# Kernel tuning notes

Hardware: AMD Instinct MI355X
Metric: run time of the kernel (lower is better)

Reference implementation:

```python
import jax, jax.numpy as jnp
import numpy as np

B, E, H, V, D2, T = 128, 512, 512, 32000, 1024, 17

def setup_inputs() -> dict:
    key = jax.random.key(0)
    ks = jax.random.split(key, 13)
    s = 0.02
    return {
        "features": jax.random.normal(ks[0], (B, 512), dtype=jnp.float32),
        "captions": jax.random.randint(ks[1], (B, T), 0, V, dtype=jnp.int32),
        "W_enc": jax.random.normal(ks[2], (512, E), dtype=jnp.float32) * s,
        "b_enc": jnp.zeros((E,), dtype=jnp.float32),
        "emb": jax.random.normal(ks[3], (V, E), dtype=jnp.float32) * s,
        "W_ih": jax.random.normal(ks[4], (4 * H, E), dtype=jnp.float32) * s,
        "b_ih": jnp.zeros((4 * H,), dtype=jnp.float32),
        "W_hh": jax.random.normal(ks[5], (4 * H, H), dtype=jnp.float32) * s,
        "b_hh": jnp.zeros((4 * H,), dtype=jnp.float32),
        "W_d2": jax.random.normal(ks[6], (H, D2), dtype=jnp.float32) * s,
        "b_d2": jnp.zeros((D2,), dtype=jnp.float32),
        "W_last": jax.random.normal(ks[7], (D2, V), dtype=jnp.float32) * s,
        "b_last": jnp.zeros((V,), dtype=jnp.float32),
    }


def reference(features, captions, W_enc, b_enc, emb, W_ih, b_ih, W_hh, b_hh, W_d2, b_d2, W_last, b_last):
    # encoder_last: project frozen-resnet features [B,512] -> [B,E]
    feat = features @ W_enc + b_enc
    # embed captions[:, :-1] -> [B,16,E], prepend image feature -> [B,17,E]
    e = emb[captions[:, :-1]]
    x = jnp.concatenate([feat[:, None, :], e], axis=1)  # [B,T,E]

    def step(carry, xt):
        h, c = carry
        gates = xt @ W_ih.T + b_ih + h @ W_hh.T + b_hh  # [B,4H]
        i, f, g, o = jnp.split(gates, 4, axis=-1)  # PyTorch LSTMCell gate order
        i, f, o = jax.nn.sigmoid(i), jax.nn.sigmoid(f), jax.nn.sigmoid(o)
        g = jnp.tanh(g)
        c = f * c + i * g
        h = o * jnp.tanh(c)
        return (h, c), h

    h0 = jnp.zeros((x.shape[0], H), dtype=x.dtype)
    c0 = jnp.zeros((x.shape[0], H), dtype=x.dtype)
    _, hs = jax.lax.scan(step, (h0, c0), jnp.swapaxes(x, 0, 1))  # [T,B,H]
    hs = jnp.swapaxes(hs, 0, 1)  # [B,T,H]

    out = jax.nn.relu(hs @ W_d2 + b_d2)       # [B,T,D2]
    logits = out @ W_last + b_last            # [B,T,V]
    return jax.nn.softmax(logits, axis=2)
```

## Files before the change

### kernel.cpp

```cpp
#include <hip/hip_runtime.h>
#include <hip/hip_bf16.h>

#define B_   128
#define T_   17
#define E_   512
#define H_   512
#define V_   32000
#define D2_  1024
#define MR_  (B_*T_)

typedef __attribute__((ext_vector_type(8))) short short8;
typedef __attribute__((ext_vector_type(4))) float f32x4;

__device__ __forceinline__ unsigned short f2b(float f) {
  unsigned u = __float_as_uint(f);
  u += 0x7FFFu + ((u >> 16) & 1u);
  return (unsigned short)(u >> 16);
}
__device__ __forceinline__ float sigf(float x) { return 1.f / (1.f + __expf(-x)); }
__device__ __forceinline__ float tanhfast(float x) {
  x = fminf(fmaxf(x, -15.f), 15.f);
  float e = __expf(2.f * x);
  return (e - 1.f) / (e + 1.f);
}

__device__ __forceinline__ void async16(const void* g, void* l) {
  __builtin_amdgcn_global_load_lds((const __attribute__((address_space(1))) unsigned int*)g,
                                   (__attribute__((address_space(3))) unsigned int*)l,
                                   16, 0, 0);
}

template<int EPI>
__global__ __launch_bounds__(256, 2)
void gemm_bt(const unsigned short* __restrict__ A,
             const unsigned short* __restrict__ Bt,
             void* __restrict__ C,
             const float* __restrict__ bias0,
             const float* __restrict__ bias1,
             int N, int K)
{
  __shared__ unsigned short sA[128 * 32];
  __shared__ unsigned short sB[128 * 32];

  const int tid  = threadIdx.x;
  const int lane = tid & 63;
  const int wave = tid >> 6;
  const int wm   = wave & 1;
  const int wn   = wave >> 1;
  const size_t bm = (size_t)blockIdx.x * 128;
  const size_t bn = (size_t)blockIdx.y * 128;

  const int sRow   = wave * 32 + (lane >> 2);
  const int gchunk = (lane & 3) ^ ((sRow >> 2) & 3);

  const unsigned short* gA  = A  + (bm + sRow)      * (size_t)K + gchunk * 8;
  const unsigned short* gA2 = A  + (bm + sRow + 16) * (size_t)K + gchunk * 8;
  const unsigned short* gB  = Bt + (bn + sRow)      * (size_t)K + gchunk * 8;
  const unsigned short* gB2 = Bt + (bn + sRow + 16) * (size_t)K + gchunk * 8;

  unsigned short* lA  = &sA[wave * 1024];
  unsigned short* lA2 = &sA[wave * 1024 + 512];
  unsigned short* lB  = &sB[wave * 1024];
  unsigned short* lB2 = &sB[wave * 1024 + 512];

  f32x4 acc[4][4] = {};
  const int fm = lane & 15;
  const int q  = lane >> 4;

  for (int kt = 0; kt < K; kt += 32) {
    async16(gA  + kt, lA);
    async16(gA2 + kt, lA2);
    async16(gB  + kt, lB);
    async16(gB2 + kt, lB2);
    __syncthreads();

    short8 af[4], bfv[4];
#pragma unroll
    for (int i = 0; i < 4; i++) {
      int ra = wm * 64 + i * 16 + fm;
      af[i]  = *(const short8*)&sA[ra * 32 + ((q ^ ((ra >> 2) & 3)) * 8)];
      int rb = wn * 64 + i * 16 + fm;
      bfv[i] = *(const short8*)&sB[rb * 32 + ((q ^ ((rb >> 2) & 3)) * 8)];
    }
#pragma unroll
    for (int i = 0; i < 4; i++)
#pragma unroll
      for (int j = 0; j < 4; j++)
        acc[i][j] = __builtin_amdgcn_mfma_f32_16x16x32_bf16(af[i], bfv[j], acc[i][j], 0, 0, 0);
    __syncthreads();
  }

#pragma unroll
  for (int i = 0; i < 4; i++) {
#pragma unroll
    for (int j = 0; j < 4; j++) {
      size_t col = bn + wn * 64 + j * 16 + fm;
      float bv = 0.f;
      if constexpr (EPI == 0) {
        size_t oc = ((col & 3) << 9) + (col >> 2);
        bv = bias0[oc] + bias1[oc];
      }
      if constexpr (EPI == 2 || EPI == 3 || EPI == 4) bv = bias0[col];
#pragma unroll
      for (int r = 0; r < 4; r++) {
        size_t row = bm + wm * 64 + i * 16 + q * 4 + r;
        float v = acc[i][j][r] + bv;
        if constexpr (EPI == 2) {
          v = v > 0.f ? v : 0.f;
          ((unsigned short*)C)[row * N + col] = f2b(v);
        } else if constexpr (EPI == 3) {
          ((unsigned short*)C)[row * N + col] = f2b(v);
        } else {
          ((float*)C)[row * N + col] = v;
        }
      }
    }
  }
}

__global__ __launch_bounds__(256)
void lstm_step(const unsigned short* __restrict__ hprev,
               const unsigned short* __restrict__ Whh,
               const float* __restrict__ Gt,
               float* __restrict__ c,
               unsigned short* __restrict__ hout,
               unsigned short* __restrict__ hsb,
               int t)
{
  __shared__ float gl[128 * 132];
  unsigned short* sA = (unsigned short*)gl;
  unsigned short* sB = (unsigned short*)(gl + 4096);

  const int tid  = threadIdx.x;
  const int lane = tid & 63;
  const int wave = tid >> 6;
  const int wm   = wave & 1;
  const int wn   = wave >> 1;
  const int n0   = blockIdx.x * 128;

  const int sR  = lane >> 3;
  const int gch = (lane & 7) ^ sR;
  const size_t aoff = (size_t)(wave * 32 + sR) * 512 + gch * 8;
  const size_t boff = (size_t)(n0 + wave * 32 + sR) * 512 + gch * 8;

  f32x4 acc[4][4] = {};
  const int fm = lane & 15;
  const int q  = lane >> 4;

  for (int kt = 0; kt < 512; kt += 64) {
#pragma unroll
    for (int s = 0; s < 4; s++) {
      async16(hprev + aoff + s * 4096 + kt, sA + wave * 2048 + s * 512);
      async16(Whh   + boff + s * 4096 + kt, sB + wave * 2048 + s * 512);
    }
    __syncthreads();

    short8 af[2][4], bfv[2][4];
#pragma unroll
    for (int kk = 0; kk < 2; kk++) {
      int cch = kk * 4 + q;
#pragma unroll
      for (int i = 0; i < 4; i++) {
        int ra = wm * 64 + i * 16 + fm;
        af[kk][i]  = *(const short8*)&sA[ra * 64 + ((cch ^ (ra & 7)) * 8)];
        int rb = wn * 64 + i * 16 + fm;
        bfv[kk][i] = *(const short8*)&sB[rb * 64 + ((cch ^ (rb & 7)) * 8)];
      }
    }
#pragma unroll
    for (int kk = 0; kk < 2; kk++)
#pragma unroll
      for (int i = 0; i < 4; i++)
#pragma unroll
        for (int j = 0; j < 4; j++)
          acc[i][j] = __builtin_amdgcn_mfma_f32_16x16x32_bf16(af[kk][i], bfv[kk][j], acc[i][j], 0, 0, 0);
    __syncthreads();
  }

#pragma unroll
  for (int i = 0; i < 4; i++)
#pragma unroll
    for (int j = 0; j < 4; j++)
#pragma unroll
      for (int r = 0; r < 4; r++)
        gl[(wm * 64 + i * 16 + q * 4 + r) * 132 + wn * 64 + j * 16 + fm] = acc[i][j][r];
  __syncthreads();

#pragma unroll
  for (int it = 0; it < 16; it++) {
    int p   = it * 256 + tid;
    int row = p >> 5;
    int ul  = p & 31;
    float4 a4 = *(float4*)&gl[row * 132 + ul * 4];
    float4 G4 = *(const float4*)&Gt[row * 2048 + n0 + ul * 4];
    float gi = a4.x + G4.x, gf = a4.y + G4.y, gg = a4.z + G4.z, go = a4.w + G4.w;
    int gu  = (n0 >> 2) + ul;
    int idx = row * 512 + gu;
    float cn = sigf(gf) * c[idx] + sigf(gi) * tanhfast(gg);
    c[idx] = cn;
    float hn = sigf(go) * tanhfast(cn);
    unsigned short h16 = f2b(hn);
    hout[idx] = h16;
    hsb[((size_t)row * T_ + t) * 512 + gu] = h16;
  }
}

__global__ void lstm_point0(const float* __restrict__ G0, float* __restrict__ c,
                            unsigned short* __restrict__ hb, unsigned short* __restrict__ hsb) {
  int idx = blockIdx.x * 256 + threadIdx.x;
  int b = idx >> 9, u = idx & 511;
  float4 g4 = ((const float4*)(G0 + (size_t)b * 2048))[u];
  float cn = sigf(g4.x) * tanhfast(g4.z);
  c[idx] = cn;
  float hn = sigf(g4.w) * tanhfast(cn);
  unsigned short h16 = f2b(hn);
  hb[idx] = h16;
  hsb[((size_t)b * T_ + 0) * 512 + u] = h16;
}

__global__ void permute_cvt(const float* __restrict__ src, unsigned short* __restrict__ dst) {
  int p  = blockIdx.x;
  int ir = ((p & 3) << 9) + (p >> 2);
  float4 v = ((const float4*)(src + (size_t)ir * 512))[threadIdx.x];
  ushort4 o;
  o.x = f2b(v.x); o.y = f2b(v.y); o.z = f2b(v.z); o.w = f2b(v.w);
  ((ushort4*)(dst + (size_t)p * 512))[threadIdx.x] = o;
}

__global__ void transpose_cvt(const float* __restrict__ src, unsigned short* __restrict__ dst,
                              int K, int N) {
  __shared__ float tile[32][33];
  int n0 = blockIdx.x * 32, k0 = blockIdx.y * 32;
  int tcol = threadIdx.x & 31, trow = threadIdx.x >> 5;
  for (int r = trow; r < 32; r += 8)
    tile[r][tcol] = src[(size_t)(k0 + r) * N + n0 + tcol];
  __syncthreads();
  for (int r = trow; r < 32; r += 8)
    dst[(size_t)(n0 + r) * K + k0 + tcol] = f2b(tile[tcol][r]);
}

__global__ __launch_bounds__(256) void encode(const float* __restrict__ features,
                                              const float* __restrict__ W_enc,
                                              const float* __restrict__ b_enc,
                                              unsigned short* __restrict__ xb) {
  __shared__ float fs[512];
  int b = blockIdx.y, e = blockIdx.x * 256 + threadIdx.x;
  fs[threadIdx.x]       = features[b * 512 + threadIdx.x];
  fs[threadIdx.x + 256] = features[b * 512 + threadIdx.x + 256];
  __syncthreads();
  float acc = 0.f;
#pragma unroll 8
  for (int k = 0; k < 512; k++) acc += fs[k] * W_enc[(size_t)k * 512 + e];
  xb[(size_t)b * 512 + e] = f2b(acc + b_enc[e]);
}

__global__ void embed_k(const int* __restrict__ captions, const float* __restrict__ emb,
                        unsigned short* __restrict__ xb) {
  int t = blockIdx.x + 1, b = blockIdx.y;
  int tok = captions[b * T_ + (t - 1)];
  float4 v = ((const float4*)(emb + (size_t)tok * 512))[threadIdx.x];
  ushort4 o;
  o.x = f2b(v.x); o.y = f2b(v.y); o.z = f2b(v.z); o.w = f2b(v.w);
  ((ushort4*)(xb + (size_t)(t * B_ + b) * 512))[threadIdx.x] = o;
}

__global__ __launch_bounds__(1024) void softmax_b(const unsigned short* __restrict__ lg,
                                                  float* __restrict__ out) {
  __shared__ float ps[1024];
  const uint4* r4 = (const uint4*)(lg + (size_t)blockIdx.x * V_);
  float* orow = out + (size_t)blockIdx.x * V_;
  int tid = threadIdx.x;
  float v[4][8];
  float s = 0.f;
#pragma unroll
  for (int u = 0; u < 4; u++) {
    int i = u * 1024 + tid;
    if (i < 4000) {
      uint4 w = r4[i];
      unsigned a[4] = {w.x, w.y, w.z, w.w};
#pragma unroll
      for (int k = 0; k < 4; k++) {
        float lo = __uint_as_float(a[k] << 16);
        float hi = __uint_as_float(a[k] & 0xffff0000u);
        float e0 = __expf(lo), e1 = __expf(hi);
        v[u][2 * k] = e0; v[u][2 * k + 1] = e1;
        s += e0 + e1;
      }
    }
  }
  ps[tid] = s;
  __syncthreads();
  for (int o = 512; o > 0; o >>= 1) {
    if (tid < o) ps[tid] += ps[tid + o];
    __syncthreads();
  }
  float inv = 1.f / ps[0];
#pragma unroll
  for (int u = 0; u < 4; u++) {
    int i = u * 1024 + tid;
    if (i < 4000) {
      float4 o1 = {v[u][0] * inv, v[u][1] * inv, v[u][2] * inv, v[u][3] * inv};
      float4 o2 = {v[u][4] * inv, v[u][5] * inv, v[u][6] * inv, v[u][7] * inv};
      ((float4*)(orow + (size_t)i * 8))[0] = o1;
      ((float4*)(orow + (size_t)i * 8))[1] = o2;
    }
  }
}

__global__ __launch_bounds__(1024) void softmax_f(float* __restrict__ out) {
  __shared__ float ps[1024];
  float* r = out + (size_t)blockIdx.x * V_;
  int tid = threadIdx.x;
  float v[32];
  float s = 0.f;
#pragma unroll
  for (int u = 0; u < 32; u++) {
    int i = u * 1024 + tid;
    if (i < V_) { float e = __expf(r[i]); v[u] = e; s += e; }
  }
  ps[tid] = s;
  __syncthreads();
  for (int o = 512; o > 0; o >>= 1) {
    if (tid < o) ps[tid] += ps[tid + o];
    __syncthreads();
  }
  float inv = 1.f / ps[0];
#pragma unroll
  for (int u = 0; u < 32; u++) {
    int i = u * 1024 + tid;
    if (i < V_) r[i] = v[u] * inv;
  }
}

extern "C" void kernel_launch(void* const* d_in, const int* in_sizes, int n_in,
                              void* d_out, int out_size, void* d_ws, size_t ws_size,
                              hipStream_t stream) {
  const float* features = (const float*)d_in[0];
  const int*   captions = (const int*)d_in[1];
  const float* W_enc  = (const float*)d_in[2];
  const float* b_enc  = (const float*)d_in[3];
  const float* emb    = (const float*)d_in[4];
  const float* W_ih   = (const float*)d_in[5];
  const float* b_ih   = (const float*)d_in[6];
  const float* W_hh   = (const float*)d_in[7];
  const float* b_hh   = (const float*)d_in[8];
  const float* W_d2   = (const float*)d_in[9];
  const float* b_d2   = (const float*)d_in[10];
  const float* W_last = (const float*)d_in[11];
  const float* b_last = (const float*)d_in[12];
  float* out = (float*)d_out;

  char* ws = (char*)d_ws;
  size_t off = 0;
  auto alloc = [&](size_t bytes) -> void* {
    void* p = ws + off;
    off += (bytes + 255) & ~(size_t)255;
    return p;
  };
  unsigned short* xb     = (unsigned short*)alloc((size_t)MR_ * E_ * 2);
  unsigned short* Wb_ih  = (unsigned short*)alloc((size_t)4 * H_ * E_ * 2);
  unsigned short* Wb_hh  = (unsigned short*)alloc((size_t)4 * H_ * H_ * 2);
  unsigned short* Wb_d2t = (unsigned short*)alloc((size_t)D2_ * H_ * 2);
  unsigned short* Wb_lt  = (unsigned short*)alloc((size_t)V_ * D2_ * 2);
  float*          G      = (float*)alloc((size_t)MR_ * 4 * H_ * 4);
  float*          cst    = (float*)alloc((size_t)B_ * H_ * 4);
  unsigned short* hb0    = (unsigned short*)alloc((size_t)B_ * H_ * 2);
  unsigned short* hb1    = (unsigned short*)alloc((size_t)B_ * H_ * 2);
  unsigned short* hsb    = (unsigned short*)alloc((size_t)MR_ * H_ * 2);
  unsigned short* outb   = (unsigned short*)alloc((size_t)MR_ * D2_ * 2);
  size_t off_base = off;
  unsigned short* lgb    = (unsigned short*)alloc((size_t)MR_ * V_ * 2);
  const bool bf16_logits = (off <= ws_size);
  (void)in_sizes; (void)n_in; (void)out_size; (void)off_base;

  permute_cvt<<<2048, 128, 0, stream>>>(W_ih, Wb_ih);
  permute_cvt<<<2048, 128, 0, stream>>>(W_hh, Wb_hh);
  transpose_cvt<<<dim3(D2_ / 32, H_ / 32), 256, 0, stream>>>(W_d2, Wb_d2t, H_, D2_);

  encode<<<dim3(2, B_), 256, 0, stream>>>(features, W_enc, b_enc, xb);
  embed_k<<<dim3(T_ - 1, B_), 128, 0, stream>>>(captions, emb, xb);

  gemm_bt<0><<<dim3(MR_ / 128, 4 * H_ / 128), 256, 0, stream>>>(xb, Wb_ih, G, b_ih, b_hh, 4 * H_, E_);

  lstm_point0<<<B_ * H_ / 256, 256, 0, stream>>>(G, cst, hb0, hsb);
  for (int t = 1; t < T_; t++) {
    unsigned short* hp = (t & 1) ? hb0 : hb1;
    unsigned short* hc = (t & 1) ? hb1 : hb0;
    lstm_step<<<16, 256, 0, stream>>>(hp, Wb_hh, G + (size_t)t * B_ * 4 * H_, cst, hc, hsb, t);
  }

  transpose_cvt<<<dim3(V_ / 32, D2_ / 32), 256, 0, stream>>>(W_last, Wb_lt, D2_, V_);

  gemm_bt<2><<<dim3(MR_ / 128, D2_ / 128), 256, 0, stream>>>(hsb, Wb_d2t, outb, b_d2, nullptr, D2_, H_);

  if (bf16_logits) {
    gemm_bt<3><<<dim3(MR_ / 128, V_ / 128), 256, 0, stream>>>(outb, Wb_lt, lgb, b_last, nullptr, V_, D2_);
    softmax_b<<<MR_, 1024, 0, stream>>>(lgb, out);
  } else {
    gemm_bt<4><<<dim3(MR_ / 128, V_ / 128), 256, 0, stream>>>(outb, Wb_lt, out, b_last, nullptr, V_, D2_);
    softmax_f<<<MR_, 1024, 0, stream>>>(out);
  }
}
```

Baseline: 973.2 us.

## Swizzle vocab GEMM blocks per XCD, deepen LSTM step K-tile, fuse weight converts

The large vocab-projection GEMM now uses a 1D grid whose block indices are remapped so each of the 8 XCDs handles a contiguous range of tiles sharing the same W_last columns, aiming for better L2 reuse. The LSTM recurrent step loads 256-wide K slices into 128 KB of LDS, so it runs 2 barrier-separated iterations instead of 8 and spends less time synchronising. The two weight permute/convert launches are merged into one. The large LDS allocation limits occupancy to one block per CU, though the step kernel only launches 16 blocks anyway.

```diff
diff --git a/kernel.cpp b/kernel.cpp
--- a/kernel.cpp
+++ b/kernel.cpp
@@ -30,25 +30,32 @@
                                    16, 0, 0);
 }
 
-template<int EPI>
+template<int EPI, int SWZ>
 __global__ __launch_bounds__(256, 2)
 void gemm_bt(const unsigned short* __restrict__ A,
              const unsigned short* __restrict__ Bt,
              void* __restrict__ C,
              const float* __restrict__ bias0,
              const float* __restrict__ bias1,
-             int N, int K)
+             int N, int K, int nbm, int nwork)
 {
   __shared__ unsigned short sA[128 * 32];
   __shared__ unsigned short sB[128 * 32];
+
+  int f = blockIdx.x;
+  if constexpr (SWZ) {
+    int per = (nwork + 7) >> 3;
+    f = (f & 7) * per + (f >> 3);
+    if (f >= nwork) return;
+  }
+  const size_t bm = (size_t)(f % nbm) * 128;
+  const size_t bn = (size_t)(f / nbm) * 128;
 
   const int tid  = threadIdx.x;
   const int lane = tid & 63;
   const int wave = tid >> 6;
   const int wm   = wave & 1;
   const int wn   = wave >> 1;
-  const size_t bm = (size_t)blockIdx.x * 128;
-  const size_t bn = (size_t)blockIdx.y * 128;
 
   const int sRow   = wave * 32 + (lane >> 2);
   const int gchunk = (lane & 3) ^ ((sRow >> 2) & 3);
@@ -127,9 +134,10 @@
                unsigned short* __restrict__ hsb,
                int t)
 {
-  __shared__ float gl[128 * 132];
-  unsigned short* sA = (unsigned short*)gl;
-  unsigned short* sB = (unsigned short*)(gl + 4096);
+  __shared__ char smem[131072];
+  unsigned short* sA = (unsigned short*)smem;
+  unsigned short* sB = (unsigned short*)(smem + 65536);
+  float* gl = (float*)smem;
 
   const int tid  = threadIdx.x;
   const int lane = tid & 63;
@@ -138,42 +146,42 @@
   const int wn   = wave >> 1;
   const int n0   = blockIdx.x * 128;
 
-  const int sR  = lane >> 3;
-  const int gch = (lane & 7) ^ sR;
-  const size_t aoff = (size_t)(wave * 32 + sR) * 512 + gch * 8;
-  const size_t boff = (size_t)(n0 + wave * 32 + sR) * 512 + gch * 8;
+  const int lr = lane >> 5;
+  const int lp = lane & 31;
 
   f32x4 acc[4][4] = {};
   const int fm = lane & 15;
   const int q  = lane >> 4;
 
-  for (int kt = 0; kt < 512; kt += 64) {
-#pragma unroll
-    for (int s = 0; s < 4; s++) {
-      async16(hprev + aoff + s * 4096 + kt, sA + wave * 2048 + s * 512);
-      async16(Whh   + boff + s * 4096 + kt, sB + wave * 2048 + s * 512);
-    }
-    __syncthreads();
-
-    short8 af[2][4], bfv[2][4];
-#pragma unroll
-    for (int kk = 0; kk < 2; kk++) {
-      int cch = kk * 4 + q;
+  for (int kt = 0; kt < 512; kt += 256) {
+#pragma unroll
+    for (int s = 0; s < 16; s++) {
+      int row = wave * 32 + s * 2 + lr;
+      int gch = lp ^ (row & 7);
+      async16(hprev + (size_t)row * 512 + kt + gch * 8,
+              sA + wave * 8192 + s * 512 + lane * 8);
+      async16(Whh + (size_t)(n0 + row) * 512 + kt + gch * 8,
+              sB + wave * 8192 + s * 512 + lane * 8);
+    }
+    __syncthreads();
+
+#pragma unroll
+    for (int kk = 0; kk < 8; kk++) {
+      int ch = kk * 4 + q;
+      short8 af[4], bfv[4];
 #pragma unroll
       for (int i = 0; i < 4; i++) {
         int ra = wm * 64 + i * 16 + fm;
-        af[kk][i]  = *(const short8*)&sA[ra * 64 + ((cch ^ (ra & 7)) * 8)];
+        af[i]  = *(const short8*)&sA[ra * 256 + ((ch ^ (ra & 7)) * 8)];
         int rb = wn * 64 + i * 16 + fm;
-        bfv[kk][i] = *(const short8*)&sB[rb * 64 + ((cch ^ (rb & 7)) * 8)];
+        bfv[i] = *(const short8*)&sB[rb * 256 + ((ch ^ (rb & 7)) * 8)];
       }
-    }
-#pragma unroll
-    for (int kk = 0; kk < 2; kk++)
 #pragma unroll
       for (int i = 0; i < 4; i++)
 #pragma unroll
         for (int j = 0; j < 4; j++)
-          acc[i][j] = __builtin_amdgcn_mfma_f32_16x16x32_bf16(af[kk][i], bfv[kk][j], acc[i][j], 0, 0, 0);
+          acc[i][j] = __builtin_amdgcn_mfma_f32_16x16x32_bf16(af[i], bfv[j], acc[i][j], 0, 0, 0);
+    }
     __syncthreads();
   }
 
@@ -218,9 +226,13 @@
   hsb[((size_t)b * T_ + 0) * 512 + u] = h16;
 }
 
-__global__ void permute_cvt(const float* __restrict__ src, unsigned short* __restrict__ dst) {
-  int p  = blockIdx.x;
-  int ir = ((p & 3) << 9) + (p >> 2);
+__global__ void permute_cvt2(const float* __restrict__ Wih, const float* __restrict__ Whh,
+                             unsigned short* __restrict__ dih, unsigned short* __restrict__ dhh) {
+  int p = blockIdx.x;
+  const float* src = (p < 2048) ? Wih : Whh;
+  unsigned short* dst = (p < 2048) ? dih : dhh;
+  int pp = p & 2047;
+  int ir = ((pp & 3) << 9) + (pp >> 2);
   float4 v = ((const float4*)(src + (size_t)ir * 512))[threadIdx.x];
   ushort4 o;
   o.x = f2b(v.x); o.y = f2b(v.y); o.z = f2b(v.z); o.w = f2b(v.w);
@@ -368,19 +380,17 @@
   unsigned short* hb1    = (unsigned short*)alloc((size_t)B_ * H_ * 2);
   unsigned short* hsb    = (unsigned short*)alloc((size_t)MR_ * H_ * 2);
   unsigned short* outb   = (unsigned short*)alloc((size_t)MR_ * D2_ * 2);
-  size_t off_base = off;
   unsigned short* lgb    = (unsigned short*)alloc((size_t)MR_ * V_ * 2);
   const bool bf16_logits = (off <= ws_size);
-  (void)in_sizes; (void)n_in; (void)out_size; (void)off_base;
-
-  permute_cvt<<<2048, 128, 0, stream>>>(W_ih, Wb_ih);
-  permute_cvt<<<2048, 128, 0, stream>>>(W_hh, Wb_hh);
+  (void)in_sizes; (void)n_in; (void)out_size;
+
+  permute_cvt2<<<4096, 128, 0, stream>>>(W_ih, W_hh, Wb_ih, Wb_hh);
   transpose_cvt<<<dim3(D2_ / 32, H_ / 32), 256, 0, stream>>>(W_d2, Wb_d2t, H_, D2_);
 
   encode<<<dim3(2, B_), 256, 0, stream>>>(features, W_enc, b_enc, xb);
   embed_k<<<dim3(T_ - 1, B_), 128, 0, stream>>>(captions, emb, xb);
 
-  gemm_bt<0><<<dim3(MR_ / 128, 4 * H_ / 128), 256, 0, stream>>>(xb, Wb_ih, G, b_ih, b_hh, 4 * H_, E_);
+  gemm_bt<0, 0><<<17 * 16, 256, 0, stream>>>(xb, Wb_ih, G, b_ih, b_hh, 4 * H_, E_, 17, 17 * 16);
 
   lstm_point0<<<B_ * H_ / 256, 256, 0, stream>>>(G, cst, hb0, hsb);
   for (int t = 1; t < T_; t++) {
@@ -391,13 +401,15 @@
 
   transpose_cvt<<<dim3(V_ / 32, D2_ / 32), 256, 0, stream>>>(W_last, Wb_lt, D2_, V_);
 
-  gemm_bt<2><<<dim3(MR_ / 128, D2_ / 128), 256, 0, stream>>>(hsb, Wb_d2t, outb, b_d2, nullptr, D2_, H_);
-
+  gemm_bt<2, 0><<<17 * 8, 256, 0, stream>>>(hsb, Wb_d2t, outb, b_d2, nullptr, D2_, H_, 17, 17 * 8);
+
+  const int nwork = 17 * (V_ / 128);
+  const int per   = (nwork + 7) / 8;
   if (bf16_logits) {
-    gemm_bt<3><<<dim3(MR_ / 128, V_ / 128), 256, 0, stream>>>(outb, Wb_lt, lgb, b_last, nullptr, V_, D2_);
+    gemm_bt<3, 1><<<8 * per, 256, 0, stream>>>(outb, Wb_lt, lgb, b_last, nullptr, V_, D2_, 17, nwork);
     softmax_b<<<MR_, 1024, 0, stream>>>(lgb, out);
   } else {
-    gemm_bt<4><<<dim3(MR_ / 128, V_ / 128), 256, 0, stream>>>(outb, Wb_lt, out, b_last, nullptr, V_, D2_);
+    gemm_bt<4, 1><<<8 * per, 256, 0, stream>>>(outb, Wb_lt, out, b_last, nullptr, V_, D2_, 17, nwork);
     softmax_f<<<MR_, 1024, 0, stream>>>(out);
   }
 }
```

New measurement: 947.8 us. 2.6% less time.
